# Kernel optimization log

Measured on AMD Instinct MI355X. Metric: run time of the kernel, lower is better.

## Reference

```python
import jax, jax.numpy as jnp
import numpy as np

INPUT_DIM = 1024
NUM_HEADS = 16
D_K = 1024
HEAD_DIM = D_K // NUM_HEADS


def setup_inputs() -> dict:
    key = jax.random.key(0)
    ks = jax.random.split(key, 9)
    s_in = 1.0 / np.sqrt(INPUT_DIM)
    s_dk = 1.0 / np.sqrt(D_K)
    return {
        "x": jax.random.normal(ks[0], (2, 2048, INPUT_DIM), dtype=jnp.float32),
        "Wq": jax.random.uniform(ks[1], (INPUT_DIM, D_K), minval=-s_in, maxval=s_in, dtype=jnp.float32),
        "bq": jax.random.uniform(ks[2], (D_K,), minval=-s_in, maxval=s_in, dtype=jnp.float32),
        "Wk": jax.random.uniform(ks[3], (INPUT_DIM, D_K), minval=-s_in, maxval=s_in, dtype=jnp.float32),
        "bk": jax.random.uniform(ks[4], (D_K,), minval=-s_in, maxval=s_in, dtype=jnp.float32),
        "Wv": jax.random.uniform(ks[5], (INPUT_DIM, D_K), minval=-s_in, maxval=s_in, dtype=jnp.float32),
        "bv": jax.random.uniform(ks[6], (D_K,), minval=-s_in, maxval=s_in, dtype=jnp.float32),
        "Wo": jax.random.uniform(ks[7], (D_K, INPUT_DIM), minval=-s_dk, maxval=s_dk, dtype=jnp.float32),
        "bo": jax.random.uniform(ks[8], (INPUT_DIM,), minval=-s_dk, maxval=s_dk, dtype=jnp.float32),
    }


def reference(x, Wq, bq, Wk, bk, Wv, bv, Wo, bo):
    B, S, _ = x.shape
    H, D = NUM_HEADS, HEAD_DIM
    # QKV projections -> [B, H, S, D]
    q = (x @ Wq + bq).reshape(B, S, H, D).transpose(0, 2, 1, 3)
    k = (x @ Wk + bk).reshape(B, S, H, D).transpose(0, 2, 1, 3)
    v = (x @ Wv + bv).reshape(B, S, H, D).transpose(0, 2, 1, 3)
    scores = jnp.einsum("bhsd,bhtd->bhst", q, k) / jnp.sqrt(jnp.asarray(D, x.dtype))
    attn = jax.nn.softmax(scores, axis=-1)
    out = jnp.einsum("bhst,bhtd->bhsd", attn, v)  # [B,H,S,D]
    out = out.transpose(0, 2, 1, 3).reshape(B, S, H * D)
    return out @ Wo + bo
```

## Files before the change

### kernel.cpp

```cpp
#include <hip/hip_runtime.h>
#include <stdint.h>

typedef _Float16 f16;
typedef f16 f16x4 __attribute__((ext_vector_type(4)));
typedef f16 f16x8 __attribute__((ext_vector_type(8)));
typedef float f32x4 __attribute__((ext_vector_type(4)));
typedef float f32x16 __attribute__((ext_vector_type(16)));

#define AS1 __attribute__((address_space(1)))
#define AS3 __attribute__((address_space(3)))

__device__ __forceinline__ void gll16(const void* g, void* l) {
  __builtin_amdgcn_global_load_lds((AS1 void*)g, (AS3 void*)l, 16, 0, 0);
}

__device__ __forceinline__ f32x4 mfma16(f16x8 a, f16x8 b, f32x4 c) {
  return __builtin_amdgcn_mfma_f32_16x16x32_f16(a, b, c, 0, 0, 0);
}
__device__ __forceinline__ f32x16 mfma32(f16x8 a, f16x8 b, f32x16 c) {
  return __builtin_amdgcn_mfma_f32_32x32x16_f16(a, b, c, 0, 0, 0);
}

__device__ __forceinline__ uint32_t pk_rtn(float a, float b) {
  union { f16 h[2]; uint32_t u; } c;
  c.h[0] = (f16)a;
  c.h[1] = (f16)b;
  return c.u;
}

__device__ __forceinline__ void pl32(uint32_t& x, uint32_t& y) {
  asm("v_permlane32_swap_b32 %0, %1" : "+v"(x), "+v"(y));
}

__device__ __forceinline__ f16x8 mk_bfrag(float e0, float e1, float e2, float e3,
                                          float e4, float e5, float e6, float e7) {
  uint32_t x0 = pk_rtn(e0, e1), y0 = pk_rtn(e4, e5);
  uint32_t x1 = pk_rtn(e2, e3), y1 = pk_rtn(e6, e7);
  pl32(x0, y0);
  pl32(x1, y1);
  union { uint32_t w[4]; f16x8 v; } u;
  u.w[0] = x0; u.w[1] = x1; u.w[2] = y0; u.w[3] = y1;
  return u.v;
}

__device__ __forceinline__ f32x16 zero16() {
  f32x16 z;
#pragma unroll
  for (int i = 0; i < 16; i++) z[i] = 0.f;
  return z;
}


__global__ __launch_bounds__(256) void pack_x_k(const float* __restrict__ x,
                                                f16* __restrict__ xh, int n) {
  int i = (blockIdx.x * 256 + threadIdx.x) * 8;
  if (i < n) {
    float4 a = *(const float4*)(x + i);
    float4 b = *(const float4*)(x + i + 4);
    f16x8 o;
    o[0] = (f16)a.x; o[1] = (f16)a.y; o[2] = (f16)a.z; o[3] = (f16)a.w;
    o[4] = (f16)b.x; o[5] = (f16)b.y; o[6] = (f16)b.z; o[7] = (f16)b.w;
    *(f16x8*)(xh + i) = o;
  }
}

__global__ __launch_bounds__(256) void pack_w_k(const float* __restrict__ Wq,
                                                const float* __restrict__ Wk,
                                                const float* __restrict__ Wv,
                                                const float* __restrict__ Wo,
                                                f16* __restrict__ Wt) {
  __shared__ f16 t[64][65];
  const float* W = (blockIdx.z == 0) ? Wq : (blockIdx.z == 1) ? Wk
                   : (blockIdx.z == 2) ? Wv : Wo;
  int n0 = blockIdx.x * 64, k0 = blockIdx.y * 64;
  int tid = threadIdx.x;
  int kr = tid >> 4;
  int nc = (tid & 15) * 4;
#pragma unroll
  for (int i = 0; i < 4; i++) {
    int k = k0 + kr + i * 16;
    float4 w = *(const float4*)(W + (size_t)k * 1024 + n0 + nc);
    t[nc + 0][kr + i * 16] = (f16)w.x;
    t[nc + 1][kr + i * 16] = (f16)w.y;
    t[nc + 2][kr + i * 16] = (f16)w.z;
    t[nc + 3][kr + i * 16] = (f16)w.w;
  }
  __syncthreads();
  int nr = tid >> 2;
  int c0 = (tid & 3) * 16;
  alignas(16) f16 tmp[16];
#pragma unroll
  for (int e = 0; e < 16; e++) tmp[e] = t[nr][c0 + e];
  f16* dst = Wt + (size_t)(blockIdx.z * 1024 + n0 + nr) * 1024 + k0 + c0;
  *(f16x8*)(dst) = *(const f16x8*)(tmp);
  *(f16x8*)(dst + 8) = *(const f16x8*)(tmp + 8);
}

__device__ __forceinline__ void gemm_main(const f16* __restrict__ A,
                                          const f16* __restrict__ B,
                                          int m0, int n0,
                                          f16* Al, f16* Bl,
                                          f32x4 acc[4][4]) {
  const int K = 1024;
  int tid = threadIdx.x;
  int lane = tid & 63, wid = tid >> 6;
  int wr = (wid >> 1) * 64, wc = (wid & 1) * 64;
#pragma unroll
  for (int mi = 0; mi < 4; mi++)
#pragma unroll
    for (int nj = 0; nj < 4; nj++) {
      f32x4 z = {0.f, 0.f, 0.f, 0.f};
      acc[mi][nj] = z;
    }
  int srow = lane >> 3;
  int sgr = (lane & 7) ^ srow;
  int lr = lane & 15, lg = lane >> 4;
  for (int kt = 0; kt < 16; ++kt) {
    __syncthreads();
#pragma unroll
    for (int q = 0; q < 4; q++) {
      int chunk = wid * 4 + q;
      int row = chunk * 8 + srow;
      gll16(A + (size_t)(m0 + row) * K + kt * 64 + sgr * 8, Al + chunk * 512);
      gll16(B + (size_t)(n0 + row) * K + kt * 64 + sgr * 8, Bl + chunk * 512);
    }
    __syncthreads();
#pragma unroll
    for (int kk = 0; kk < 2; kk++) {
      f16x8 af[4], bf[4];
#pragma unroll
      for (int mi = 0; mi < 4; mi++) {
        int row = wr + mi * 16 + lr;
        int gr = (kk * 4 + lg) ^ (row & 7);
        af[mi] = *(const f16x8*)(Al + row * 64 + gr * 8);
      }
#pragma unroll
      for (int nj = 0; nj < 4; nj++) {
        int row = wc + nj * 16 + lr;
        int gr = (kk * 4 + lg) ^ (row & 7);
        bf[nj] = *(const f16x8*)(Bl + row * 64 + gr * 8);
      }
#pragma unroll
      for (int mi = 0; mi < 4; mi++)
#pragma unroll
        for (int nj = 0; nj < 4; nj++)
          acc[mi][nj] = mfma16(af[mi], bf[nj], acc[mi][nj]);
    }
  }
}

__global__ __launch_bounds__(256) void gemm_qkv_k(const f16* __restrict__ Xh,
                                                  const f16* __restrict__ Wt,
                                                  const float* __restrict__ bq,
                                                  const float* __restrict__ bk,
                                                  const float* __restrict__ bv,
                                                  f16* __restrict__ Q,
                                                  f16* __restrict__ Kb,
                                                  f16* __restrict__ Vt) {
  __shared__ f16 Al[128 * 64];
  __shared__ f16 Bl[128 * 64];
  f32x4 acc[4][4];
  int m0 = blockIdx.y * 128, n0 = blockIdx.x * 128;
  gemm_main(Xh, Wt, m0, n0, Al, Bl, acc);

  int lane = threadIdx.x & 63, wid = threadIdx.x >> 6;
  int wr = (wid >> 1) * 64, wc = (wid & 1) * 64;
  int lg = lane >> 4, lc = lane & 15;
  int which = n0 >> 10;
  if (which == 2) {
#pragma unroll
    for (int mi = 0; mi < 4; mi++)
#pragma unroll
      for (int nj = 0; nj < 4; nj++) {
        int nh = (n0 + wc + nj * 16 + lc) & 1023;
        int h = nh >> 6, d = nh & 63;
        float bb = bv[nh];
        int mbase = m0 + wr + mi * 16 + lg * 4;
        int b = mbase >> 11, s = mbase & 2047;
        f16x4 vv;
#pragma unroll
        for (int r = 0; r < 4; r++) vv[r] = (f16)(acc[mi][nj][r] + bb);
        *(f16x4*)(Vt + ((size_t)(b * 16 + h) * 64 + d) * 2048 + s) = vv;
      }
  } else {
    const float* bias = (which == 0) ? bq : bk;
    f16* out = (which == 0) ? Q : Kb;
    float scale = (which == 0) ? 0.1803368801111204f : 1.0f;
#pragma unroll
    for (int mi = 0; mi < 4; mi++)
#pragma unroll
      for (int nj = 0; nj < 4; nj++) {
        int nh = (n0 + wc + nj * 16 + lc) & 1023;
        int h = nh >> 6, d = nh & 63;
        float bb = bias[nh];
#pragma unroll
        for (int r = 0; r < 4; r++) {
          int m = m0 + wr + mi * 16 + lg * 4 + r;
          int b = m >> 11, s = m & 2047;
          float v = (acc[mi][nj][r] + bb) * scale;
          out[((size_t)(b * 16 + h) * 2048 + s) * 64 + d] = (f16)v;
        }
      }
  }
}

__global__ __launch_bounds__(256) void gemm_out_k(const f16* __restrict__ Oh,
                                                  const f16* __restrict__ Wt,
                                                  const float* __restrict__ bo,
                                                  float* __restrict__ out) {
  __shared__ f16 Al[128 * 64];
  __shared__ f16 Bl[128 * 64];
  f32x4 acc[4][4];
  int m0 = blockIdx.y * 128, n0 = blockIdx.x * 128;
  gemm_main(Oh, Wt, m0, n0, Al, Bl, acc);

  int lane = threadIdx.x & 63, wid = threadIdx.x >> 6;
  int wr = (wid >> 1) * 64, wc = (wid & 1) * 64;
  int lg = lane >> 4, lc = lane & 15;
#pragma unroll
  for (int mi = 0; mi < 4; mi++)
#pragma unroll
    for (int nj = 0; nj < 4; nj++) {
      int n = n0 + wc + nj * 16 + lc;
      float bb = bo[n];
#pragma unroll
      for (int r = 0; r < 4; r++) {
        int m = m0 + wr + mi * 16 + lg * 4 + r;
        out[(size_t)m * 1024 + n] = acc[mi][nj][r] + bb;
      }
    }
}

__global__ __launch_bounds__(256, 4) void attn_k(const f16* __restrict__ Q,
                                                 const f16* __restrict__ K,
                                                 const f16* __restrict__ Vt,
                                                 f16* __restrict__ Oh) {
  __shared__ alignas(16) char lds_raw[32768];
  f16* Kl = (f16*)lds_raw;
  f16* Vl = (f16*)(lds_raw + 16384);

  int tid = threadIdx.x, lane = tid & 63, wid = tid >> 6;
  int q5 = lane & 31, hi = lane >> 5;
  int qc2 = wid >> 1, hv = wid & 1;
  int b0 = blockIdx.x;
  int qc = (b0 >> 3) & 31;
  int bh = (b0 & 7) + ((b0 >> 8) << 3);
  int q0w = qc * 64 + qc2 * 32;

  const f16* Qp = Q + (size_t)bh * 2048 * 64;
  const f16* Kp = K + (size_t)bh * 2048 * 64;
  const f16* Vp = Vt + (size_t)bh * 64 * 2048;

  f16x8 qf[4];
  {
    const f16* qr = Qp + (size_t)(q0w + q5) * 64 + hi * 8;
#pragma unroll
    for (int ks = 0; ks < 4; ks++) qf[ks] = *(const f16x8*)(qr + ks * 16);
  }

  f32x16 o0 = zero16(), o1 = zero16();
  float lsum = 0.f;

  int srow8 = lane >> 3, swz8 = ((lane & 7) ^ srow8) * 8;
  int ch0 = wid * 2;
  const f16* sK = Kp + (size_t)(ch0 * 8 + srow8) * 64 + swz8;
  const f16* sV = Vp + (size_t)(ch0 * 8 + srow8) * 2048 + swz8;

  auto STAGE = [&](int buf, int t) {
    const f16* k = sK + (size_t)t * 4096;
    const f16* v = sV + t * 64;
    f16* dk = Kl + buf * 4096 + ch0 * 512;
    f16* dv = Vl + buf * 4096 + ch0 * 512;
    gll16(k, dk);
    gll16(k + 8 * 64, dk + 512);
    gll16(v, dv);
    gll16(v + (size_t)8 * 2048, dv + 512);
  };

  int kqoff[4];
#pragma unroll
  for (int ks = 0; ks < 4; ks++)
    kqoff[ks] = (hv * 32 + q5) * 64 + (((2 * ks + hi) ^ (q5 & 7)) << 3);
  int r0 = q5, r1 = q5 + 32;
  int voff0[2], voff1[2];
#pragma unroll
  for (int ks = 0; ks < 2; ks++) {
    voff0[ks] = r0 * 64 + (((hv * 4 + 2 * ks + hi) ^ (r0 & 7)) << 3);
    voff1[ks] = r1 * 64 + (((hv * 4 + 2 * ks + hi) ^ (r1 & 7)) << 3);
  }

  STAGE(0, 0);

  for (int t = 0; t < 32; ++t) {
    int cur = t & 1;
    if (t < 31) {
      STAGE(cur ^ 1, t + 1);
      asm volatile("s_waitcnt vmcnt(4)" ::: "memory");
    } else {
      asm volatile("s_waitcnt vmcnt(0)" ::: "memory");
    }
    __builtin_amdgcn_s_barrier();

    const f16* kb = Kl + cur * 4096;
    const f16* vb = Vl + cur * 4096;

    f32x16 s = zero16();
    __builtin_amdgcn_s_setprio(1);
#pragma unroll
    for (int ks = 0; ks < 4; ks++)
      s = mfma32(*(const f16x8*)(kb + kqoff[ks]), qf[ks], s);
    __builtin_amdgcn_s_setprio(0);

    f16x8 vf0[2], vf1[2];
#pragma unroll
    for (int ks = 0; ks < 2; ks++) {
      vf0[ks] = *(const f16x8*)(vb + voff0[ks]);
      vf1[ks] = *(const f16x8*)(vb + voff1[ks]);
    }

    float sA = 0.f, sB = 0.f, sC = 0.f, sD = 0.f;
#pragma unroll
    for (int i = 0; i < 4; i++)  { s[i] = __builtin_amdgcn_exp2f(s[i]);  sA += s[i]; }
#pragma unroll
    for (int i = 4; i < 8; i++)  { s[i] = __builtin_amdgcn_exp2f(s[i]);  sB += s[i]; }
#pragma unroll
    for (int i = 8; i < 12; i++) { s[i] = __builtin_amdgcn_exp2f(s[i]);  sC += s[i]; }
#pragma unroll
    for (int i = 12; i < 16; i++){ s[i] = __builtin_amdgcn_exp2f(s[i]);  sD += s[i]; }
    float sum = (sA + sB) + (sC + sD);
    sum += __shfl_xor(sum, 32);
    lsum += sum;

    f16x8 pb0 = mk_bfrag(s[0], s[1], s[2], s[3], s[4], s[5], s[6], s[7]);
    f16x8 pb1 = mk_bfrag(s[8], s[9], s[10], s[11], s[12], s[13], s[14], s[15]);

    __builtin_amdgcn_s_setprio(1);
    o0 = mfma32(vf0[0], pb0, o0);
    o0 = mfma32(vf0[1], pb1, o0);
    o1 = mfma32(vf1[0], pb0, o1);
    o1 = mfma32(vf1[1], pb1, o1);
    __builtin_amdgcn_s_setprio(0);

    asm volatile("" ::: "memory");
    __builtin_amdgcn_s_barrier();
  }

  __syncthreads();
  float* Ox = (float*)lds_raw + qc2 * (32 * 68);
  float* ml = (float*)lds_raw + 2 * (32 * 68) + qc2 * 32;
  if (hv == 1) {
#pragma unroll
    for (int g = 0; g < 4; g++) {
      f32x4 a, b;
#pragma unroll
      for (int j = 0; j < 4; j++) { a[j] = o0[4 * g + j]; b[j] = o1[4 * g + j]; }
      *(f32x4*)(Ox + q5 * 68 + 8 * g + 4 * hi) = a;
      *(f32x4*)(Ox + q5 * 68 + 32 + 8 * g + 4 * hi) = b;
    }
    if (hi == 0) ml[q5] = lsum;
  }
  __syncthreads();
  if (hv == 0) {
    float inv = 1.f / (lsum + ml[q5]);
    int bB = bh >> 4, hh = bh & 15;
    f16* op = Oh + ((size_t)(bB * 2048 + q0w + q5)) * 1024 + hh * 64;
#pragma unroll
    for (int g = 0; g < 4; g++) {
      f32x4 x0 = *(const f32x4*)(Ox + q5 * 68 + 8 * g + 4 * hi);
      f32x4 x1 = *(const f32x4*)(Ox + q5 * 68 + 32 + 8 * g + 4 * hi);
      f16x4 y0, y1;
#pragma unroll
      for (int j = 0; j < 4; j++) {
        y0[j] = (f16)((o0[4 * g + j] + x0[j]) * inv);
        y1[j] = (f16)((o1[4 * g + j] + x1[j]) * inv);
      }
      int d0 = 8 * g + 4 * hi;
      *(f16x4*)(op + d0) = y0;
      *(f16x4*)(op + 32 + d0) = y1;
    }
  }
}


extern "C" void kernel_launch(void* const* d_in, const int* in_sizes, int n_in,
                              void* d_out, int out_size, void* d_ws, size_t ws_size,
                              hipStream_t stream) {
  const float* x  = (const float*)d_in[0];
  const float* Wq = (const float*)d_in[1];
  const float* bq = (const float*)d_in[2];
  const float* Wk = (const float*)d_in[3];
  const float* bk = (const float*)d_in[4];
  const float* Wv = (const float*)d_in[5];
  const float* bv = (const float*)d_in[6];
  const float* Wo = (const float*)d_in[7];
  const float* bo = (const float*)d_in[8];
  float* out = (float*)d_out;

  char* ws = (char*)d_ws;
  const size_t MB8 = (size_t)8 << 20;
  f16* Xh = (f16*)(ws + 0 * MB8);
  f16* Wt = (f16*)(ws + 1 * MB8);
  f16* Q  = (f16*)(ws + 2 * MB8);
  f16* Kb = (f16*)(ws + 3 * MB8);
  f16* Vt = (f16*)(ws + 4 * MB8);
  f16* Oh = (f16*)(ws + 5 * MB8);

  pack_x_k<<<dim3(2048), dim3(256), 0, stream>>>(x, Xh, 4096 * 1024);
  pack_w_k<<<dim3(16, 16, 4), dim3(256), 0, stream>>>(Wq, Wk, Wv, Wo, Wt);
  gemm_qkv_k<<<dim3(24, 32), dim3(256), 0, stream>>>(Xh, Wt, bq, bk, bv, Q, Kb, Vt);
  attn_k<<<dim3(1024), dim3(256), 0, stream>>>(Q, Kb, Vt, Oh);
  gemm_out_k<<<dim3(8, 32), dim3(256), 0, stream>>>(Oh, Wt + (size_t)3072 * 1024, bo, out);
}
```

Measured before the change: 128.5 us.

## Narrow output GEMM tile, compute softmax row sums via MFMA, restructure attention pipeline

The output projection GEMM now uses 128x64 tiles with its own inline load/MFMA loop, doubling the grid to 512 blocks to fill more CUs. In attention, the per-row exp-sum reduction (VALU adds plus a cross-lane shuffle) is replaced by an extra MFMA against a ones vector. The double-buffer schedule changes to wait for all loads, barrier, then issue the next stage, and the trailing barrier is dropped. This trades VALU and shuffle work for MFMA work, but the full vmcnt(0) wait may reduce overlap between loads and compute.

```diff
diff --git a/kernel.cpp b/kernel.cpp
--- a/kernel.cpp
+++ b/kernel.cpp
@@ -209,23 +209,68 @@
                                                   const float* __restrict__ bo,
                                                   float* __restrict__ out) {
   __shared__ f16 Al[128 * 64];
-  __shared__ f16 Bl[128 * 64];
-  f32x4 acc[4][4];
-  int m0 = blockIdx.y * 128, n0 = blockIdx.x * 128;
-  gemm_main(Oh, Wt, m0, n0, Al, Bl, acc);
-
-  int lane = threadIdx.x & 63, wid = threadIdx.x >> 6;
-  int wr = (wid >> 1) * 64, wc = (wid & 1) * 64;
-  int lg = lane >> 4, lc = lane & 15;
+  __shared__ f16 Bl[64 * 64];
+  const int K = 1024;
+  int tid = threadIdx.x, lane = tid & 63, wid = tid >> 6;
+  int wr = (wid >> 1) * 64, wc = (wid & 1) * 32;
+  f32x4 acc[4][2];
 #pragma unroll
   for (int mi = 0; mi < 4; mi++)
 #pragma unroll
-    for (int nj = 0; nj < 4; nj++) {
+    for (int nj = 0; nj < 2; nj++) {
+      f32x4 z = {0.f, 0.f, 0.f, 0.f};
+      acc[mi][nj] = z;
+    }
+  int m0 = blockIdx.y * 128, n0 = blockIdx.x * 64;
+  int srow = lane >> 3, sgr = (lane & 7) ^ srow;
+  int lr = lane & 15, lg = lane >> 4;
+  for (int kt = 0; kt < 16; ++kt) {
+    __syncthreads();
+#pragma unroll
+    for (int q = 0; q < 4; q++) {
+      int chunk = wid * 4 + q;
+      int row = chunk * 8 + srow;
+      gll16(Oh + (size_t)(m0 + row) * K + kt * 64 + sgr * 8, Al + chunk * 512);
+    }
+#pragma unroll
+    for (int q = 0; q < 2; q++) {
+      int chunk = wid * 2 + q;
+      int row = chunk * 8 + srow;
+      gll16(Wt + (size_t)(n0 + row) * K + kt * 64 + sgr * 8, Bl + chunk * 512);
+    }
+    __syncthreads();
+#pragma unroll
+    for (int kk = 0; kk < 2; kk++) {
+      f16x8 af[4], bf[2];
+#pragma unroll
+      for (int mi = 0; mi < 4; mi++) {
+        int row = wr + mi * 16 + lr;
+        int gr = (kk * 4 + lg) ^ (row & 7);
+        af[mi] = *(const f16x8*)(Al + row * 64 + gr * 8);
+      }
+#pragma unroll
+      for (int nj = 0; nj < 2; nj++) {
+        int row = wc + nj * 16 + lr;
+        int gr = (kk * 4 + lg) ^ (row & 7);
+        bf[nj] = *(const f16x8*)(Bl + row * 64 + gr * 8);
+      }
+#pragma unroll
+      for (int mi = 0; mi < 4; mi++)
+#pragma unroll
+        for (int nj = 0; nj < 2; nj++)
+          acc[mi][nj] = mfma16(af[mi], bf[nj], acc[mi][nj]);
+    }
+  }
+  int lg4 = lg * 4, lc = lane & 15;
+#pragma unroll
+  for (int mi = 0; mi < 4; mi++)
+#pragma unroll
+    for (int nj = 0; nj < 2; nj++) {
       int n = n0 + wc + nj * 16 + lc;
       float bb = bo[n];
 #pragma unroll
       for (int r = 0; r < 4; r++) {
-        int m = m0 + wr + mi * 16 + lg * 4 + r;
+        int m = m0 + wr + mi * 16 + lg4 + r;
         out[(size_t)m * 1024 + n] = acc[mi][nj][r] + bb;
       }
     }
@@ -258,8 +303,12 @@
     for (int ks = 0; ks < 4; ks++) qf[ks] = *(const f16x8*)(qr + ks * 16);
   }
 
-  f32x16 o0 = zero16(), o1 = zero16();
-  float lsum = 0.f;
+  const f32x16 Z = zero16();
+  f16x8 ones;
+#pragma unroll
+  for (int i = 0; i < 8; i++) ones[i] = (f16)1.0f;
+
+  f32x16 o0 = Z, o1 = Z, osum = Z;
 
   int srow8 = lane >> 3, swz8 = ((lane & 7) ^ srow8) * 8;
   int ch0 = wid * 2;
@@ -293,22 +342,18 @@
 
   for (int t = 0; t < 32; ++t) {
     int cur = t & 1;
-    if (t < 31) {
-      STAGE(cur ^ 1, t + 1);
-      asm volatile("s_waitcnt vmcnt(4)" ::: "memory");
-    } else {
-      asm volatile("s_waitcnt vmcnt(0)" ::: "memory");
-    }
+    asm volatile("s_waitcnt vmcnt(0)" ::: "memory");
     __builtin_amdgcn_s_barrier();
+    if (t < 31) STAGE(cur ^ 1, t + 1);
 
     const f16* kb = Kl + cur * 4096;
     const f16* vb = Vl + cur * 4096;
 
-    f32x16 s = zero16();
     __builtin_amdgcn_s_setprio(1);
-#pragma unroll
-    for (int ks = 0; ks < 4; ks++)
-      s = mfma32(*(const f16x8*)(kb + kqoff[ks]), qf[ks], s);
+    f32x16 s = mfma32(*(const f16x8*)(kb + kqoff[0]), qf[0], Z);
+    s = mfma32(*(const f16x8*)(kb + kqoff[1]), qf[1], s);
+    s = mfma32(*(const f16x8*)(kb + kqoff[2]), qf[2], s);
+    s = mfma32(*(const f16x8*)(kb + kqoff[3]), qf[3], s);
     __builtin_amdgcn_s_setprio(0);
 
     f16x8 vf0[2], vf1[2];
@@ -318,18 +363,8 @@
       vf1[ks] = *(const f16x8*)(vb + voff1[ks]);
     }
 
-    float sA = 0.f, sB = 0.f, sC = 0.f, sD = 0.f;
-#pragma unroll
-    for (int i = 0; i < 4; i++)  { s[i] = __builtin_amdgcn_exp2f(s[i]);  sA += s[i]; }
-#pragma unroll
-    for (int i = 4; i < 8; i++)  { s[i] = __builtin_amdgcn_exp2f(s[i]);  sB += s[i]; }
-#pragma unroll
-    for (int i = 8; i < 12; i++) { s[i] = __builtin_amdgcn_exp2f(s[i]);  sC += s[i]; }
-#pragma unroll
-    for (int i = 12; i < 16; i++){ s[i] = __builtin_amdgcn_exp2f(s[i]);  sD += s[i]; }
-    float sum = (sA + sB) + (sC + sD);
-    sum += __shfl_xor(sum, 32);
-    lsum += sum;
+#pragma unroll
+    for (int i = 0; i < 16; i++) s[i] = __builtin_amdgcn_exp2f(s[i]);
 
     f16x8 pb0 = mk_bfrag(s[0], s[1], s[2], s[3], s[4], s[5], s[6], s[7]);
     f16x8 pb1 = mk_bfrag(s[8], s[9], s[10], s[11], s[12], s[13], s[14], s[15]);
@@ -339,11 +374,12 @@
     o0 = mfma32(vf0[1], pb1, o0);
     o1 = mfma32(vf1[0], pb0, o1);
     o1 = mfma32(vf1[1], pb1, o1);
+    osum = mfma32(ones, pb0, osum);
+    osum = mfma32(ones, pb1, osum);
     __builtin_amdgcn_s_setprio(0);
-
-    asm volatile("" ::: "memory");
-    __builtin_amdgcn_s_barrier();
-  }
+  }
+
+  float lsum = osum[0];
 
   __syncthreads();
   float* Ox = (float*)lds_raw + qc2 * (32 * 68);
@@ -409,5 +445,5 @@
   pack_w_k<<<dim3(16, 16, 4), dim3(256), 0, stream>>>(Wq, Wk, Wv, Wo, Wt);
   gemm_qkv_k<<<dim3(24, 32), dim3(256), 0, stream>>>(Xh, Wt, bq, bk, bv, Q, Kb, Vt);
   attn_k<<<dim3(1024), dim3(256), 0, stream>>>(Q, Kb, Vt, Oh);
-  gemm_out_k<<<dim3(8, 32), dim3(256), 0, stream>>>(Oh, Wt + (size_t)3072 * 1024, bo, out);
-}
+  gemm_out_k<<<dim3(16, 32), dim3(256), 0, stream>>>(Oh, Wt + (size_t)3072 * 1024, bo, out);
+}
```

After: 123.4 us, median of 3. -4.0%, faster.
